# Performance work log

Hardware: AMD Instinct MI355X
Metric: run time of the kernel (lower is better)

## Reference

```python
import jax, jax.numpy as jnp
import numpy as np

B, M, T, H = 32, 2048, 8, 64  # batch, measurements, num_tags, hidden_dim
LATENT, TRIL = 3, 6
NEG_INF = -1e9  # masked-out logit value for segment softmax


def _linear_init(key, fan_in, fan_out):
    # torch nn.Linear default: U(-1/sqrt(fan_in), 1/sqrt(fan_in)) for W and b
    bound = 1.0 / np.sqrt(fan_in)
    kw, kb = jax.random.split(key)
    w = jax.random.uniform(kw, (fan_in, fan_out), minval=-bound, maxval=bound, dtype=jnp.float32)
    b = jax.random.uniform(kb, (fan_out,), minval=-bound, maxval=bound, dtype=jnp.float32)
    return w, b


def setup_inputs() -> dict:
    key = jax.random.key(0)
    ks = jax.random.split(key, 14)
    inp = {}
    inp['measurements'] = jax.random.normal(ks[0], (B, M, 5), dtype=jnp.float32)
    inp['measurement_to_tag_mapping'] = jax.random.randint(ks[1], (B, M), 0, T, dtype=jnp.int32)
    inp['me_w1'], inp['me_b1'] = _linear_init(ks[2], 5, H)
    inp['me_w2'], inp['me_b2'] = _linear_init(ks[3], H, H)
    inp['q_w'], inp['q_b'] = _linear_init(ks[4], H, H)
    inp['k_w'], inp['k_b'] = _linear_init(ks[5], H, H)
    inp['v_w'], inp['v_b'] = _linear_init(ks[6], H, H)
    inp['a1_w1'], inp['a1_b1'] = _linear_init(ks[7], H, H // 2)
    inp['a1_w2'], inp['a1_b2'] = _linear_init(ks[8], H // 2, 1)
    inp['a2_w1'], inp['a2_b1'] = _linear_init(ks[9], H, H // 2)
    inp['a2_w2'], inp['a2_b2'] = _linear_init(ks[10], H // 2, 1)
    inp['mu_w'], inp['mu_b'] = _linear_init(ks[11], H, LATENT)
    inp['logL_w'], inp['logL_b'] = _linear_init(ks[12], H, TRIL)
    return inp


def reference(measurements, measurement_to_tag_mapping,
              me_w1, me_b1, me_w2, me_b2,
              q_w, q_b, k_w, k_b, v_w, v_b,
              a1_w1, a1_b1, a1_w2, a1_b2,
              a2_w1, a2_b1, a2_w2, a2_b2,
              mu_w, mu_b, logL_w, logL_b):
    # measurement encoder: two Linear+ReLU layers -> [B, M, H]
    feat = jax.nn.relu(measurements @ me_w1 + me_b1)
    feat = jax.nn.relu(feat @ me_w2 + me_b2)

    # self-attention with residual
    q = feat @ q_w + q_b
    k = feat @ k_w + k_b
    v = feat @ v_w + v_b
    scale = jnp.sqrt(jnp.float32(H))
    scores = jnp.einsum('bmh,bnh->bmn', q, k) / scale  # [B, M, M]
    feat = feat + jnp.einsum('bmn,bnh->bmh', jax.nn.softmax(scores, axis=-1), v)

    # per-measurement attention logits (attention_net1) -> [B, M]
    a1 = (jax.nn.relu(feat @ a1_w1 + a1_b1) @ a1_w2 + a1_b2)[..., 0]

    # segment softmax per tag id: mask [B, M, T]
    tag_mask = measurement_to_tag_mapping[..., None] == jnp.arange(T)
    seg_logits = jnp.where(tag_mask, a1[..., None], NEG_INF)
    seg_w = jax.nn.softmax(seg_logits, axis=1)  # softmax over measurements within each tag
    tag_feat = jnp.einsum('bmt,bmh->bth', seg_w, feat)  # [B, T, H]

    # aggregate tags (attention_net2) -> pose feature [B, H]
    a2 = (jax.nn.relu(tag_feat @ a2_w1 + a2_b1) @ a2_w2 + a2_b2)[..., 0]  # [B, T]
    tag_w = jax.nn.softmax(a2, axis=-1)
    pose = jnp.einsum('bt,bth->bh', tag_w, tag_feat)

    mu = pose @ mu_w + mu_b
    logL = pose @ logL_w + logL_b
    return mu, logL
```

## Files before the change

### kernel.cpp

```cpp
#include <hip/hip_runtime.h>
#include <hip/hip_bf16.h>
#include <cstdint>
#include <cstddef>


typedef short s16x8 __attribute__((ext_vector_type(8)));
typedef float f32x4 __attribute__((ext_vector_type(4)));
typedef float f32x16 __attribute__((ext_vector_type(16)));

#define LOG2E  1.4426950408889634f
#define QSCALE 0.18033688011112042f

__device__ __forceinline__ unsigned short f2bf(float f) {
    unsigned u = __builtin_bit_cast(unsigned, f);
    u += 0x7fffu + ((u >> 16) & 1u);
    return (unsigned short)(u >> 16);
}

__device__ __forceinline__ unsigned cvtpk(float lo, float hi) {
    unsigned r;
    asm("v_cvt_pk_bf16_f32 %0, %1, %2" : "=v"(r) : "v"(lo), "v"(hi));
    return r;
}

__device__ __forceinline__ float exp2_raw(float x) {
    float r;
    asm("v_exp_f32 %0, %1" : "=v"(r) : "v"(x));
    return r;
}

#define PLSWAP(a, b) asm("v_permlane32_swap_b32 %0, %1" : "+v"(a), "+v"(b))

__device__ __forceinline__ void gload_lds16(const void* g, void* l) {
    __builtin_amdgcn_global_load_lds((const __attribute__((address_space(1))) void*)g,
                                     (__attribute__((address_space(3))) void*)l, 16, 0, 0);
}

#define MFMA16(a, b, c) __builtin_amdgcn_mfma_f32_16x16x32_bf16((a), (b), (c), 0, 0, 0)
#define MFMA32(a, b, c) __builtin_amdgcn_mfma_f32_32x32x16_bf16((a), (b), (c), 0, 0, 0)

__global__ void k_prep(const float* __restrict__ w2, const float* __restrict__ qw,
                       const float* __restrict__ kw, const float* __restrict__ vw,
                       unsigned short* __restrict__ wt)
{
    int tid = blockIdx.x * 256 + threadIdx.x;
    for (int idx = tid; idx < 4096; idx += 2048) {
        int o = idx >> 6, i = idx & 63;
        wt[idx]         = f2bf(w2[i * 64 + o]);
        wt[4096 + idx]  = f2bf(qw[i * 64 + o] * QSCALE);
        wt[8192 + idx]  = f2bf(kw[i * 64 + o]);
        wt[12288 + idx] = f2bf(vw[i * 64 + o]);
    }
}

__global__ __launch_bounds__(256)
void k_encode(const float* __restrict__ meas, const float* __restrict__ w1,
              const float* __restrict__ b1, const float* __restrict__ b2,
              const float* __restrict__ qb, const float* __restrict__ kb,
              const float* __restrict__ vb,
              const unsigned short* __restrict__ wt,
              float* __restrict__ feat,
              unsigned short* __restrict__ qbf, unsigned short* __restrict__ kbf,
              unsigned short* __restrict__ vt)
{
    __shared__ __align__(16) unsigned short hbuf[4][1152];
    int tid = threadIdx.x;
    int w = tid >> 6, lane = tid & 63;
    int g = lane >> 4, c16 = lane & 15;
    int m0 = (blockIdx.x * 4 + w) * 16;
    int b  = m0 >> 11;
    unsigned short* hb = hbuf[w];
    int vrow = lane >> 2, vseg = lane & 3;

    float x[5];
    const float* xr = meas + (size_t)(m0 + c16) * 5;
#pragma unroll
    for (int i = 0; i < 5; ++i) x[i] = xr[i];
    s16x8 aH[2];
#pragma unroll
    for (int s = 0; s < 2; ++s) {
#pragma unroll
        for (int jj = 0; jj < 8; ++jj) {
            int j = 8 * g + jj + 32 * s;
            float acc = b1[j];
#pragma unroll
            for (int i = 0; i < 5; ++i) acc += x[i] * w1[i * 64 + j];
            aH[s][jj] = (short)f2bf(fmaxf(acc, 0.f));
        }
    }

    const f32x4 zero = {0.f, 0.f, 0.f, 0.f};
    f32x4 c[4];

#pragma unroll
    for (int dt = 0; dt < 4; ++dt) {
        c[dt] = zero;
#pragma unroll
        for (int s = 0; s < 2; ++s) {
            s16x8 bf = *(const s16x8*)(wt + (c16 + 16 * dt) * 64 + 32 * s + 8 * g);
            c[dt] = MFMA16(aH[s], bf, c[dt]);
        }
    }
#pragma unroll
    for (int dt = 0; dt < 4; ++dt) {
        int d = c16 + 16 * dt;
        float bias = b2[d];
#pragma unroll
        for (int r = 0; r < 4; ++r) {
            float v = fmaxf(c[dt][r] + bias, 0.f);
            feat[(size_t)(m0 + 4 * g + r) * 64 + d] = v;
            hb[(4 * g + r) * 72 + d] = f2bf(v);
        }
    }
    s16x8 aF[2];
#pragma unroll
    for (int s = 0; s < 2; ++s)
        aF[s] = *(const s16x8*)(hb + c16 * 72 + 32 * s + 8 * g);

    auto gemmW = [&](const unsigned short* wmat, f32x4* cc) {
#pragma unroll
        for (int dt = 0; dt < 4; ++dt) {
            cc[dt] = zero;
#pragma unroll
            for (int s = 0; s < 2; ++s) {
                s16x8 bf = *(const s16x8*)(wmat + (c16 + 16 * dt) * 64 + 32 * s + 8 * g);
                cc[dt] = MFMA16(aF[s], bf, cc[dt]);
            }
        }
    };
    auto storeV = [&](const float* bias4, unsigned short* dstbase) {
#pragma unroll
        for (int dt = 0; dt < 4; ++dt) {
            int d = c16 + 16 * dt;
#pragma unroll
            for (int r = 0; r < 4; ++r)
                hb[(4 * g + r) * 72 + d] = f2bf(c[dt][r] + bias4[dt]);
        }
        s16x8 o0 = *(const s16x8*)(hb + vrow * 72 + vseg * 16);
        s16x8 o1 = *(const s16x8*)(hb + vrow * 72 + vseg * 16 + 8);
        unsigned short* dst = dstbase + (size_t)(m0 + vrow) * 64 + vseg * 16;
        *(s16x8*)dst = o0;
        *(s16x8*)(dst + 8) = o1;
    };

    float bias4[4];
    gemmW(wt + 4096, c);
#pragma unroll
    for (int dt = 0; dt < 4; ++dt) bias4[dt] = qb[c16 + 16 * dt] * QSCALE;
    storeV(bias4, qbf);
    gemmW(wt + 8192, c);
#pragma unroll
    for (int dt = 0; dt < 4; ++dt) bias4[dt] = kb[c16 + 16 * dt];
    storeV(bias4, kbf);
    gemmW(wt + 12288, c);
#pragma unroll
    for (int dt = 0; dt < 4; ++dt) {
        int d = c16 + 16 * dt;
        float bias = vb[d];
#pragma unroll
        for (int r = 0; r < 4; ++r)
            hb[(4 * g + r) * 72 + d] = f2bf(c[dt][r] + bias);
    }
    unsigned short tvv[16];
#pragma unroll
    for (int mr = 0; mr < 16; ++mr) tvv[mr] = hb[mr * 72 + lane];
    s16x8 v0, v1;
#pragma unroll
    for (int e2 = 0; e2 < 8; ++e2) { v0[e2] = (short)tvv[e2]; v1[e2] = (short)tvv[8 + e2]; }
    unsigned short* dst = vt + ((size_t)b * 64 + lane) * 2048 + (m0 & 2047);
    *(s16x8*)dst = v0;
    *(s16x8*)(dst + 8) = v1;
}

__global__ __launch_bounds__(512, 4)
void k_attn(const unsigned short* __restrict__ qbf, const unsigned short* __restrict__ kbf,
            const unsigned short* __restrict__ vt, float* __restrict__ feat)
{
    __shared__ __align__(16) char smem[37888];

    int tid = threadIdx.x;
    int w_ = tid >> 6, lane = tid & 63;
    int h = lane >> 5, c32 = lane & 31;
    int jhalf = w_ & 1, tile = w_ >> 1;
    int bid = (int)blockIdx.x;
    bid = (bid & 7) * 64 + (bid >> 3);
    int b = bid >> 4;
    int q0g = (bid & 15) * 128 + tile * 32;
    size_t rowbase = (size_t)b * 2048;

    const unsigned short* kbf_b = kbf + rowbase * 64;
    const unsigned short* vt_b  = vt + (size_t)b * 64 * 2048;

    s16x8 qf[4];
    {
        const unsigned short* qp = qbf + (rowbase + q0g + c32) * 64 + 8 * h;
#pragma unroll
        for (int st = 0; st < 4; ++st)
            qf[st] = *(const s16x8*)(qp + 16 * st);
    }

    f32x16 zero16;
#pragma unroll
    for (int i = 0; i < 16; ++i) zero16[i] = 0.f;

    f32x16 o[2];
#pragma unroll
    for (int dt = 0; dt < 2; ++dt)
#pragma unroll
        for (int i = 0; i < 16; ++i) o[dt][i] = 0.f;
    float ll = 0.f;

    int srow = 8 * w_ + (lane >> 3);
    int scol = (lane & 7) ^ (srow & 7);
    const unsigned short* gk0 = kbf_b + (size_t)srow * 64 + scol * 8;
    const unsigned short* gv0 = vt_b + (size_t)srow * 2048 + scol * 8;

    auto stage = [&](int kt, int buf) {
        gload_lds16(gk0 + (size_t)kt * 4096, smem + buf * 8192 + w_ * 1024);
        gload_lds16(gv0 + kt * 64, smem + 16384 + buf * 8192 + w_ * 1024);
    };

    stage(0, 0);
    __syncthreads();

    int swz = c32 & 7;
    int krow = 32 * jhalf + c32;

    for (int kt = 0; kt < 32; ++kt) {
        int cur = kt & 1;
        if (kt + 1 < 32) stage(kt + 1, cur ^ 1);

        const char* Kb = smem + cur * 8192;
        const char* Vb = smem + 16384 + cur * 8192;

        s16x8 kf[4], vf[2][2];
#pragma unroll
        for (int st = 0; st < 4; ++st)
            kf[st] = *(const s16x8*)(Kb + krow * 128 + (((2 * st + h) ^ swz) * 16));
#pragma unroll
        for (int ks = 0; ks < 2; ++ks)
#pragma unroll
            for (int dt = 0; dt < 2; ++dt)
                vf[ks][dt] = *(const s16x8*)(Vb + (32 * dt + c32) * 128 +
                                             (((4 * jhalf + 2 * ks + h) ^ swz) * 16));

        __builtin_amdgcn_s_setprio(1);
        f32x16 sc = MFMA32(kf[0], qf[0], zero16);
#pragma unroll
        for (int st = 1; st < 4; ++st)
            sc = MFMA32(kf[st], qf[st], sc);
        __builtin_amdgcn_s_setprio(0);

        float p[16];
#pragma unroll
        for (int i = 0; i < 16; ++i) p[i] = exp2_raw(sc[i]);

        float s;
        {
            float a0 = p[0] + p[1],  a1 = p[2] + p[3],  a2 = p[4] + p[5],  a3 = p[6] + p[7];
            float a4 = p[8] + p[9],  a5 = p[10] + p[11], a6 = p[12] + p[13], a7 = p[14] + p[15];
            float b0 = a0 + a1, b1 = a2 + a3, b2 = a4 + a5, b3 = a6 + a7;
            s = (b0 + b1) + (b2 + b3);
        }
        {
            float s1 = s, s2 = s;
            PLSWAP(s1, s2);
            s = s1 + s2;
        }
        ll += s;

        unsigned u[8];
#pragma unroll
        for (int k2 = 0; k2 < 8; ++k2) u[k2] = cvtpk(p[2 * k2], p[2 * k2 + 1]);

        __builtin_amdgcn_s_setprio(1);
#pragma unroll
        for (int ks = 0; ks < 2; ++ks) {
            unsigned a0 = u[4 * ks + 0], b0 = u[4 * ks + 2];
            unsigned a1 = u[4 * ks + 1], b1 = u[4 * ks + 3];
            PLSWAP(a0, b0);
            PLSWAP(a1, b1);
            union { unsigned uu[4]; s16x8 v; } pa;
            pa.uu[0] = a0; pa.uu[1] = a1; pa.uu[2] = b0; pa.uu[3] = b1;
#pragma unroll
            for (int dt = 0; dt < 2; ++dt)
                o[dt] = MFMA32(pa.v, vf[ks][dt], o[dt]);
        }
        __builtin_amdgcn_s_setprio(0);
        __syncthreads();
    }

    float* Om = (float*)smem;
    float* Ml = (float*)(smem + 36864);
    if (jhalf) {
#pragma unroll
        for (int dt = 0; dt < 2; ++dt)
#pragma unroll
            for (int rg = 0; rg < 4; ++rg) {
                f32x4 vv;
#pragma unroll
                for (int r = 0; r < 4; ++r) vv[r] = o[dt][4 * rg + r];
                *(f32x4*)&Om[(tile * 64 + 32 * dt + c32) * 36 + 8 * rg + 4 * h] = vv;
            }
        if (h == 0) Ml[tile * 32 + c32] = ll;
    }
    __syncthreads();
    if (!jhalf) {
        float l1 = Ml[tile * 32 + c32];
        float f = 1.f / (ll + l1);
        float fr[16];
#pragma unroll
        for (int r = 0; r < 16; ++r) {
            int qrow = (r & 3) + 8 * (r >> 2) + 4 * h;
            fr[r] = __shfl(f, qrow);
        }
#pragma unroll
        for (int dt = 0; dt < 2; ++dt)
#pragma unroll
            for (int rg = 0; rg < 4; ++rg) {
                f32x4 pv = *(const f32x4*)&Om[(tile * 64 + 32 * dt + c32) * 36 + 8 * rg + 4 * h];
#pragma unroll
                for (int r = 0; r < 4; ++r) {
                    int rr = 4 * rg + r;
                    int qrow = r + 8 * rg + 4 * h;
                    size_t fi = (rowbase + q0g + qrow) * 64 + 32 * dt + c32;
                    feat[fi] += (o[dt][rr] + pv[r]) * fr[rr];
                }
            }
    }
}

__global__ __launch_bounds__(256)
void k_a1tag(const float* __restrict__ feat, const int* __restrict__ map,
             const float* __restrict__ a1w1, const float* __restrict__ b1,
             const float* __restrict__ w2, const float* __restrict__ b2,
             float* __restrict__ part1, float* __restrict__ part0)
{
    __shared__ float psum[128][33];
    __shared__ float es[128];
    __shared__ float accv[4][8][64];
    __shared__ float s0red[4][8];

    int b = blockIdx.x >> 4;
    int c = blockIdx.x & 15;
    int tid = threadIdx.x, lane = tid & 63, w = tid >> 6;
    int m0 = c * 128;
    const int* mp = map + b * 2048 + m0;
    const float* fbase = feat + ((size_t)b * 2048 + m0) * 64;

    {
        int r = tid & 127, kh = tid >> 7;
        const float* fr = fbase + (size_t)r * 64 + kh * 32;
        float acc[32];
#pragma unroll
        for (int j = 0; j < 32; ++j) acc[j] = kh ? 0.f : b1[j];
#pragma unroll
        for (int kk = 0; kk < 32; ++kk) {
            float fv = fr[kk];
            const float* wr = a1w1 + (kh * 32 + kk) * 32;
#pragma unroll
            for (int j = 0; j < 32; ++j)
                acc[j] = fmaf(fv, wr[j], acc[j]);
        }
        if (kh) {
#pragma unroll
            for (int j = 0; j < 32; ++j) psum[r][j] = acc[j];
        }
        __syncthreads();
        if (!kh) {
            float s = b2[0];
#pragma unroll
            for (int j = 0; j < 32; ++j)
                s += fmaxf(acc[j] + psum[r][j], 0.f) * w2[j];
            es[r] = exp2_raw(s * LOG2E);
        }
    }
    __syncthreads();

    float tacc[8], s0t[8];
#pragma unroll
    for (int t = 0; t < 8; ++t) { tacc[t] = 0.f; s0t[t] = 0.f; }
    for (int mi = w; mi < 128; mi += 4) {
        int tg = mp[mi];
        float e = es[mi];
        float wf = e * fbase[(size_t)mi * 64 + lane];
#pragma unroll
        for (int t = 0; t < 8; ++t)
            if (tg == t) { tacc[t] += wf; s0t[t] += e; }
    }
#pragma unroll
    for (int t = 0; t < 8; ++t) accv[w][t][lane] = tacc[t];
    if (lane == 0) {
#pragma unroll
        for (int t = 0; t < 8; ++t) s0red[w][t] = s0t[t];
    }
    __syncthreads();
    for (int e = tid; e < 512; e += 256) {
        int t = e >> 6, d = e & 63;
        part1[((size_t)c * 32 + b) * 512 + e] =
            accv[0][t][d] + accv[1][t][d] + accv[2][t][d] + accv[3][t][d];
    }
    if (tid < 8)
        part0[((size_t)c * 32 + b) * 8 + tid] =
            s0red[0][tid] + s0red[1][tid] + s0red[2][tid] + s0red[3][tid];
}

__global__ __launch_bounds__(256)
void k_head(const float* __restrict__ part1, const float* __restrict__ part0,
            const float* __restrict__ a2w1, const float* __restrict__ a2b1,
            const float* __restrict__ a2w2, const float* __restrict__ a2b2,
            const float* __restrict__ muw, const float* __restrict__ mub,
            const float* __restrict__ lLw, const float* __restrict__ lLb,
            float* __restrict__ out)
{
    __shared__ float tf[8][64];
    __shared__ float deni[8];
    __shared__ float sc8[8];
    __shared__ float pose[64];
    int b = blockIdx.x;
    int tid = threadIdx.x;

    if (tid < 8) {
        float s = 0.f;
#pragma unroll
        for (int c = 0; c < 16; ++c) s += part0[((size_t)c * 32 + b) * 8 + tid];
        deni[tid] = 1.f / s;
    }
    __syncthreads();
    for (int e = tid; e < 512; e += 256) {
        float s = 0.f;
#pragma unroll
        for (int c = 0; c < 16; ++c) s += part1[((size_t)c * 32 + b) * 512 + e];
        tf[e >> 6][e & 63] = s * deni[e >> 6];
    }
    __syncthreads();

    {
        int t = tid >> 5, j = tid & 31;
        float acc = a2b1[j];
        for (int d = 0; d < 64; ++d) acc += tf[t][d] * a2w1[d * 32 + j];
        float hsum = fmaxf(acc, 0.f) * a2w2[j];
        hsum += __shfl_xor(hsum, 1);
        hsum += __shfl_xor(hsum, 2);
        hsum += __shfl_xor(hsum, 4);
        hsum += __shfl_xor(hsum, 8);
        hsum += __shfl_xor(hsum, 16);
        if (j == 0) sc8[t] = hsum + a2b2[0];
    }
    __syncthreads();
    if (tid < 64) {
        float smax = sc8[0];
#pragma unroll
        for (int t = 1; t < 8; ++t) smax = fmaxf(smax, sc8[t]);
        float e[8], ssum = 0.f;
#pragma unroll
        for (int t = 0; t < 8; ++t) { e[t] = exp2f((sc8[t] - smax) * LOG2E); ssum += e[t]; }
        float rinv = 1.f / ssum;
        float p = 0.f;
#pragma unroll
        for (int t = 0; t < 8; ++t) p += (e[t] * rinv) * tf[t][tid];
        pose[tid] = p;
    }
    __syncthreads();
    if (tid < 3) {
        float acc = mub[tid];
        for (int d = 0; d < 64; ++d) acc += pose[d] * muw[d * 3 + tid];
        out[b * 3 + tid] = acc;
    }
    if (tid >= 32 && tid < 38) {
        int oo = tid - 32;
        float acc = lLb[oo];
        for (int d = 0; d < 64; ++d) acc += pose[d] * lLw[d * 6 + oo];
        out[96 + b * 6 + oo] = acc;
    }
}

extern "C" void kernel_launch(void* const* d_in, const int* in_sizes, int n_in,
                              void* d_out, int out_size, void* d_ws, size_t ws_size,
                              hipStream_t stream)
{
    (void)in_sizes; (void)n_in; (void)out_size; (void)ws_size;

    const float* measurements = (const float*)d_in[0];
    const int*   mapping      = (const int*)d_in[1];
    const float* me_w1 = (const float*)d_in[2];
    const float* me_b1 = (const float*)d_in[3];
    const float* me_w2 = (const float*)d_in[4];
    const float* me_b2 = (const float*)d_in[5];
    const float* q_w   = (const float*)d_in[6];
    const float* q_b   = (const float*)d_in[7];
    const float* k_w   = (const float*)d_in[8];
    const float* k_b   = (const float*)d_in[9];
    const float* v_w   = (const float*)d_in[10];
    const float* v_b   = (const float*)d_in[11];
    const float* a1_w1 = (const float*)d_in[12];
    const float* a1_b1 = (const float*)d_in[13];
    const float* a1_w2 = (const float*)d_in[14];
    const float* a1_b2 = (const float*)d_in[15];
    const float* a2_w1 = (const float*)d_in[16];
    const float* a2_b1 = (const float*)d_in[17];
    const float* a2_w2 = (const float*)d_in[18];
    const float* a2_b2 = (const float*)d_in[19];
    const float* mu_w  = (const float*)d_in[20];
    const float* mu_b  = (const float*)d_in[21];
    const float* logL_w = (const float*)d_in[22];
    const float* logL_b = (const float*)d_in[23];

    char* ws = (char*)d_ws;
    unsigned short* wt    = (unsigned short*)(ws);
    float*          feat  = (float*)(ws + 40960);
    unsigned short* qbf   = (unsigned short*)(ws + 16818176);
    unsigned short* kbf   = (unsigned short*)(ws + 25206784);
    unsigned short* vt    = (unsigned short*)(ws + 33595392);
    float*          part1 = (float*)(ws + 42248192);
    float*          part0 = (float*)(ws + 43296768);
    float*          out   = (float*)d_out;

    k_prep<<<8, 256, 0, stream>>>(me_w2, q_w, k_w, v_w, wt);
    k_encode<<<1024, 256, 0, stream>>>(measurements, me_w1, me_b1, me_b2, q_b, k_b, v_b,
                                       wt, feat, qbf, kbf, vt);
    k_attn<<<512, 512, 0, stream>>>(qbf, kbf, vt, feat);
    k_a1tag<<<512, 256, 0, stream>>>(feat, mapping, a1_w1, a1_b1, a1_w2, a1_b2,
                                     part1, part0);
    k_head<<<32, 256, 0, stream>>>(part1, part0, a2_w1, a2_b1, a2_w2, a2_b2,
                                   mu_w, mu_b, logL_w, logL_b, out);
}
```

Before: 110.8 us.

## Triple-buffer K/V staging in attention kernel and vectorize feature loads in logits kernel

After: 111.6 us. Within noise of the previous version (+0.7%).

```diff
diff --git a/kernel.cpp b/kernel.cpp
--- a/kernel.cpp
+++ b/kernel.cpp
@@ -30,6 +30,11 @@
 }
 
 #define PLSWAP(a, b) asm("v_permlane32_swap_b32 %0, %1" : "+v"(a), "+v"(b))
+
+#define WAITBAR(N) do { \
+    asm volatile("s_waitcnt vmcnt(" #N ")\n\ts_barrier" ::: "memory"); \
+    __builtin_amdgcn_sched_barrier(0); \
+} while (0)
 
 __device__ __forceinline__ void gload_lds16(const void* g, void* l) {
     __builtin_amdgcn_global_load_lds((const __attribute__((address_space(1))) void*)g,
@@ -176,7 +181,7 @@
 void k_attn(const unsigned short* __restrict__ qbf, const unsigned short* __restrict__ kbf,
             const unsigned short* __restrict__ vt, float* __restrict__ feat)
 {
-    __shared__ __align__(16) char smem[37888];
+    __shared__ __align__(16) char smem[49152];
 
     int tid = threadIdx.x;
     int w_ = tid >> 6, lane = tid & 63;
@@ -217,21 +222,15 @@
 
     auto stage = [&](int kt, int buf) {
         gload_lds16(gk0 + (size_t)kt * 4096, smem + buf * 8192 + w_ * 1024);
-        gload_lds16(gv0 + kt * 64, smem + 16384 + buf * 8192 + w_ * 1024);
+        gload_lds16(gv0 + kt * 64, smem + 24576 + buf * 8192 + w_ * 1024);
     };
-
-    stage(0, 0);
-    __syncthreads();
 
     int swz = c32 & 7;
     int krow = 32 * jhalf + c32;
 
-    for (int kt = 0; kt < 32; ++kt) {
-        int cur = kt & 1;
-        if (kt + 1 < 32) stage(kt + 1, cur ^ 1);
-
-        const char* Kb = smem + cur * 8192;
-        const char* Vb = smem + 16384 + cur * 8192;
+    auto compute = [&](int buf) {
+        const char* Kb = smem + buf * 8192;
+        const char* Vb = smem + 24576 + buf * 8192;
 
         s16x8 kf[4], vf[2][2];
 #pragma unroll
@@ -287,8 +286,22 @@
                 o[dt] = MFMA32(pa.v, vf[ks][dt], o[dt]);
         }
         __builtin_amdgcn_s_setprio(0);
-        __syncthreads();
-    }
+    };
+
+    stage(0, 0);
+    stage(1, 1);
+    WAITBAR(2);
+
+#pragma unroll 3
+    for (int kt = 0; kt < 30; ++kt) {
+        stage(kt + 2, (kt + 2) % 3);
+        compute(kt % 3);
+        WAITBAR(2);
+    }
+    compute(0);
+    WAITBAR(0);
+    compute(1);
+    __syncthreads();
 
     float* Om = (float*)smem;
     float* Ml = (float*)(smem + 36864);
@@ -350,17 +363,20 @@
 
     {
         int r = tid & 127, kh = tid >> 7;
-        const float* fr = fbase + (size_t)r * 64 + kh * 32;
+        const f32x4* fr4 = (const f32x4*)(fbase + (size_t)r * 64 + kh * 32);
         float acc[32];
 #pragma unroll
         for (int j = 0; j < 32; ++j) acc[j] = kh ? 0.f : b1[j];
 #pragma unroll
-        for (int kk = 0; kk < 32; ++kk) {
-            float fv = fr[kk];
-            const float* wr = a1w1 + (kh * 32 + kk) * 32;
-#pragma unroll
-            for (int j = 0; j < 32; ++j)
-                acc[j] = fmaf(fv, wr[j], acc[j]);
+        for (int kc = 0; kc < 8; ++kc) {
+            f32x4 fv = fr4[kc];
+#pragma unroll
+            for (int ki = 0; ki < 4; ++ki) {
+                const float* wr = a1w1 + (kh * 32 + kc * 4 + ki) * 32;
+#pragma unroll
+                for (int j = 0; j < 32; ++j)
+                    acc[j] = fmaf(fv[ki], wr[j], acc[j]);
+            }
         }
         if (kh) {
 #pragma unroll
```
